# Kernel tuning notes

Hardware: AMD Instinct MI355X
Metric: run time of the kernel (lower is better)

Reference implementation:

```python
import jax, jax.numpy as jnp
import numpy as np
from jax import lax

B, N, C = 4, 4096, 512
HEADS, SR = 8, 4
HW = 64  # spatial size, HW*HW == N
EPS = 1e-5


def setup_inputs() -> dict:
    key = jax.random.key(0)
    ks = jax.random.split(key, 12)
    s = 0.02
    return {
        "x": jax.random.normal(ks[0], (B, N, C), jnp.float32),
        "wq": jax.random.normal(ks[1], (C, C), jnp.float32) * s,
        "bq": jnp.zeros((C,), jnp.float32),
        "wk": jax.random.normal(ks[2], (C, C), jnp.float32) * s,
        "bk": jnp.zeros((C,), jnp.float32),
        "wv": jax.random.normal(ks[3], (C, C), jnp.float32) * s,
        "bv": jnp.zeros((C,), jnp.float32),
        "w_sr": jax.random.normal(ks[4], (SR, SR, C, C), jnp.float32) * s,  # HWIO
        "b_sr": jnp.zeros((C,), jnp.float32),
        "gamma": jnp.ones((C,), jnp.float32),
        "beta": jnp.zeros((C,), jnp.float32),
        "wp": jax.random.normal(ks[5], (C, C), jnp.float32) * s,
        "bp": jnp.zeros((C,), jnp.float32),
    }


def _layernorm(x, gamma, beta):
    mu = jnp.mean(x, axis=-1, keepdims=True)
    var = jnp.mean(jnp.square(x - mu), axis=-1, keepdims=True)
    return (x - mu) * lax.rsqrt(var + EPS) * gamma + beta


def reference(x, wq, bq, wk, bk, wv, bv, w_sr, b_sr, gamma, beta, wp, bp):
    b, n, c = x.shape
    dh = c // HEADS
    scale = dh ** (-0.5)
    # Q at full resolution: [b, heads, n, dh]
    q = (x @ wq + bq).reshape(b, n, HEADS, dh).transpose(0, 2, 1, 3)
    # spatial reduction of K/V: conv stride=kernel=SR (VALID)
    xr = x.reshape(b, HW, HW, c)
    xr = lax.conv_general_dilated(
        xr, w_sr, window_strides=(SR, SR), padding="VALID",
        dimension_numbers=("NHWC", "HWIO", "NHWC")) + b_sr
    xr = xr.reshape(b, -1, c)  # [b, n_kv, c]
    xr = _layernorm(xr, gamma, beta)
    n_kv = xr.shape[1]
    k = (xr @ wk + bk).reshape(b, n_kv, HEADS, dh).transpose(0, 2, 1, 3)
    v = (xr @ wv + bv).reshape(b, n_kv, HEADS, dh).transpose(0, 2, 1, 3)
    attn = jnp.einsum("bhqd,bhkd->bhqk", q, k) * scale
    attn = jax.nn.softmax(attn, axis=-1)
    out = jnp.einsum("bhqk,bhkd->bhqd", attn, v)
    out = out.transpose(0, 2, 1, 3).reshape(b, n, c)
    return out @ wp + bp
```

## Files before the change

### kernel.cpp

```cpp
#include <hip/hip_runtime.h>
#include <hip/hip_bf16.h>


#define EPSV 1e-5f

typedef __attribute__((ext_vector_type(8))) short short8v;
typedef __attribute__((ext_vector_type(4))) short short4v;
typedef __attribute__((ext_vector_type(4))) float float4v;

static __device__ __forceinline__ ushort f2bf_bits(float x) {
  union { float f; uint32_t u; } v; v.f = x;
  return (ushort)((v.u + 0x7fffu + ((v.u >> 16) & 1u)) >> 16);
}

static __device__ __forceinline__ float4v mfma16(short8v a, short8v b, float4v c) {
  return __builtin_amdgcn_mfma_f32_16x16x32_bf16(a, b, c, 0, 0, 0);
}

static __device__ __forceinline__ void wr_chunk(ushort* lds, int base, int4 v) {
  *(int2*)&lds[base]       = make_int2(v.x, v.y);
  *(int2*)&lds[base + 128] = make_int2(v.z, v.w);
}

__global__ __launch_bounds__(256) void cast_x(const float* __restrict__ src,
                                              ushort* __restrict__ dst) {
  const int i = blockIdx.x * 256 + threadIdx.x;
  const float4* s4 = (const float4*)src;
  const float4 a = s4[2 * i], b = s4[2 * i + 1];
  short8v v;
  v[0] = (short)f2bf_bits(a.x); v[1] = (short)f2bf_bits(a.y);
  v[2] = (short)f2bf_bits(a.z); v[3] = (short)f2bf_bits(a.w);
  v[4] = (short)f2bf_bits(b.x); v[5] = (short)f2bf_bits(b.y);
  v[6] = (short)f2bf_bits(b.z); v[7] = (short)f2bf_bits(b.w);
  *(short8v*)&dst[(size_t)i * 8] = v;
}

__global__ __launch_bounds__(256) void tcast(const float* __restrict__ src,
                                             ushort* __restrict__ dst, int K) {
  const int t = blockIdx.x * 256 + threadIdx.x;
  const int k = t >> 7, n4 = (t & 127) * 4;
  const float4 v = *(const float4*)&src[(size_t)k * 512 + n4];
  dst[(size_t)(n4 + 0) * K + k] = f2bf_bits(v.x);
  dst[(size_t)(n4 + 1) * K + k] = f2bf_bits(v.y);
  dst[(size_t)(n4 + 2) * K + k] = f2bf_bits(v.z);
  dst[(size_t)(n4 + 3) * K + k] = f2bf_bits(v.w);
}

__global__ __launch_bounds__(256) void concat_bias(const float* __restrict__ bk,
                                                   const float* __restrict__ bv,
                                                   float* __restrict__ bkv) {
  const int i = blockIdx.x * 256 + threadIdx.x;
  bkv[i] = (i < 512) ? bk[i] : bv[i - 512];
}

template<int MODE>
__global__ __launch_bounds__(256)
void gemm_bf(const ushort* __restrict__ A, const ushort* __restrict__ BT,
             const float* __restrict__ bias, void* __restrict__ outp,
             int M, int N, int K, float scale) {
  __shared__ ushort lds[8192];
  const int tid = threadIdx.x;
  const int wave = tid >> 6, lane = tid & 63;
  const int wm = wave >> 1, wn = wave & 1;
  const int bm = blockIdx.x * 128, bn = blockIdx.y * 128;
  const int lid = lane & 15, lg = lane >> 4;
  const int r0 = tid >> 2, c8 = tid & 3;
  const int g0 = 2 * (c8 & 1), h2 = c8 >> 1;
  const int c0 = c8 * 8;
  const int basew = ((r0 >> 4) * 64 + 16 * g0 + (r0 & 15)) * 8 + h2 * 4;
  float4v acc[4][4];
  const float4v zf = {0.f, 0.f, 0.f, 0.f};
#pragma unroll
  for (int mi = 0; mi < 4; ++mi)
#pragma unroll
    for (int ni = 0; ni < 4; ++ni) acc[mi][ni] = zf;
  const ushort* Ar0 = A + (size_t)(bm + r0) * K;
  const ushort* Ar1 = Ar0 + (size_t)64 * K;
  const ushort* Br0 = BT + (size_t)(bn + r0) * K;
  const ushort* Br1 = Br0 + (size_t)64 * K;
  const int NK = K >> 5;
  int koff = c0;
  int4 pa0 = *(const int4*)(Ar0 + koff), pa1 = *(const int4*)(Ar1 + koff);
  int4 pb0 = *(const int4*)(Br0 + koff), pb1 = *(const int4*)(Br1 + koff);
  for (int kb = 0; kb < NK; ++kb) {
    wr_chunk(lds, basew, pa0);
    wr_chunk(lds, basew + 2048, pa1);
    wr_chunk(lds, basew + 4096, pb0);
    wr_chunk(lds, basew + 6144, pb1);
    __syncthreads();
    if (kb + 1 < NK) {
      koff += 32;
      pa0 = *(const int4*)(Ar0 + koff); pa1 = *(const int4*)(Ar1 + koff);
      pb0 = *(const int4*)(Br0 + koff); pb1 = *(const int4*)(Br1 + koff);
    }
    short8v af[4], bfr[4];
#pragma unroll
    for (int mi = 0; mi < 4; ++mi)
      af[mi] = *(const short8v*)&lds[((wm * 4 + mi) * 64 + lane) * 8];
#pragma unroll
    for (int ni = 0; ni < 4; ++ni)
      bfr[ni] = *(const short8v*)&lds[4096 + ((wn * 4 + ni) * 64 + lane) * 8];
#pragma unroll
    for (int mi = 0; mi < 4; ++mi)
#pragma unroll
      for (int ni = 0; ni < 4; ++ni) acc[mi][ni] = mfma16(af[mi], bfr[ni], acc[mi][ni]);
    __syncthreads();
  }
  float bv[4];
#pragma unroll
  for (int ni = 0; ni < 4; ++ni) bv[ni] = bias[bn + wn * 64 + ni * 16 + lid];
#pragma unroll
  for (int mi = 0; mi < 4; ++mi)
#pragma unroll
    for (int ni = 0; ni < 4; ++ni) {
      const int col = bn + wn * 64 + ni * 16 + lid;
#pragma unroll
      for (int reg = 0; reg < 4; ++reg) {
        const int row = bm + wm * 64 + mi * 16 + 4 * lg + reg;
        const float v = (acc[mi][ni][reg] + bv[ni]) * scale;
        if (MODE == 0) ((float*)outp)[(size_t)row * N + col] = v;
        else if (MODE == 1) ((ushort*)outp)[(size_t)row * N + col] = f2bf_bits(v);
        else {
          if (col < 512) ((ushort*)outp)[(size_t)row * 512 + col] = f2bf_bits(v);
          else ((ushort*)outp)[524288 + (size_t)(col - 512) * 1024 + row] = f2bf_bits(v);
        }
      }
    }
}

static __device__ __forceinline__ int4 ld_patch(const ushort* xbf, int b, int oh, int ow, int kg) {
  const int ij = kg >> 9, ci = kg & 511;
  const int n = (oh * 4 + (ij >> 2)) * 64 + ow * 4 + (ij & 3);
  return *(const int4*)(xbf + ((size_t)b * 4096 + n) * 512 + ci);
}

__global__ __launch_bounds__(256)
void conv_bf(const ushort* __restrict__ xbf, const ushort* __restrict__ wsrT,
             float* __restrict__ part) {
  __shared__ ushort lds[8192];
  const int tid = threadIdx.x;
  const int wave = tid >> 6, lane = tid & 63;
  const int wm = wave >> 1, wn = wave & 1;
  const int bm = blockIdx.x * 128, bn = blockIdx.y * 128, z = blockIdx.z;
  const int lid = lane & 15, lg = lane >> 4;
  const int r0 = tid >> 2, c8 = tid & 3;
  const int g0 = 2 * (c8 & 1), h2 = c8 >> 1;
  const int c0 = c8 * 8;
  const int basew = ((r0 >> 4) * 64 + 16 * g0 + (r0 & 15)) * 8 + h2 * 4;
  const int p0 = bm + r0, p1 = p0 + 64;
  const int b0 = p0 >> 8, oh0 = (p0 & 255) >> 4, ow0 = p0 & 15;
  const int b1 = p1 >> 8, oh1 = (p1 & 255) >> 4, ow1 = p1 & 15;
  const ushort* Br0 = wsrT + (size_t)(bn + r0) * 8192;
  const ushort* Br1 = Br0 + (size_t)64 * 8192;
  float4v acc[4][4];
  const float4v zf = {0.f, 0.f, 0.f, 0.f};
#pragma unroll
  for (int mi = 0; mi < 4; ++mi)
#pragma unroll
    for (int ni = 0; ni < 4; ++ni) acc[mi][ni] = zf;
  int kg = z * 1024 + c0;
  int4 pa0 = ld_patch(xbf, b0, oh0, ow0, kg);
  int4 pa1 = ld_patch(xbf, b1, oh1, ow1, kg);
  int4 pb0 = *(const int4*)(Br0 + kg);
  int4 pb1 = *(const int4*)(Br1 + kg);
  for (int kb = 0; kb < 32; ++kb) {
    wr_chunk(lds, basew, pa0);
    wr_chunk(lds, basew + 2048, pa1);
    wr_chunk(lds, basew + 4096, pb0);
    wr_chunk(lds, basew + 6144, pb1);
    __syncthreads();
    if (kb < 31) {
      kg += 32;
      pa0 = ld_patch(xbf, b0, oh0, ow0, kg);
      pa1 = ld_patch(xbf, b1, oh1, ow1, kg);
      pb0 = *(const int4*)(Br0 + kg);
      pb1 = *(const int4*)(Br1 + kg);
    }
    short8v af[4], bfr[4];
#pragma unroll
    for (int mi = 0; mi < 4; ++mi)
      af[mi] = *(const short8v*)&lds[((wm * 4 + mi) * 64 + lane) * 8];
#pragma unroll
    for (int ni = 0; ni < 4; ++ni)
      bfr[ni] = *(const short8v*)&lds[4096 + ((wn * 4 + ni) * 64 + lane) * 8];
#pragma unroll
    for (int mi = 0; mi < 4; ++mi)
#pragma unroll
      for (int ni = 0; ni < 4; ++ni) acc[mi][ni] = mfma16(af[mi], bfr[ni], acc[mi][ni]);
    __syncthreads();
  }
#pragma unroll
  for (int mi = 0; mi < 4; ++mi)
#pragma unroll
    for (int ni = 0; ni < 4; ++ni)
#pragma unroll
      for (int reg = 0; reg < 4; ++reg)
        part[(size_t)(z * 1024 + bm + wm * 64 + mi * 16 + 4 * lg + reg) * 512 +
             bn + wn * 64 + ni * 16 + lid] = acc[mi][ni][reg];
}

__global__ __launch_bounds__(256)
void reduce_ln(const float* __restrict__ part, const float* __restrict__ bsr,
               const float* __restrict__ gamma, const float* __restrict__ beta,
               ushort* __restrict__ xln) {
  const int wave = threadIdx.x >> 6;
  const int lane = threadIdx.x & 63;
  const int row = blockIdx.x * 4 + wave;
  const int c = lane * 8;
  float v[8];
  {
    const float4 a = *(const float4*)&bsr[c];
    const float4 b = *(const float4*)&bsr[c + 4];
    v[0] = a.x; v[1] = a.y; v[2] = a.z; v[3] = a.w;
    v[4] = b.x; v[5] = b.y; v[6] = b.z; v[7] = b.w;
  }
#pragma unroll
  for (int z = 0; z < 8; ++z) {
    const float* pr = &part[((size_t)z * 1024 + row) * 512 + c];
    const float4 a = *(const float4*)pr;
    const float4 b = *(const float4*)(pr + 4);
    v[0] += a.x; v[1] += a.y; v[2] += a.z; v[3] += a.w;
    v[4] += b.x; v[5] += b.y; v[6] += b.z; v[7] += b.w;
  }
  float sum = 0.f;
#pragma unroll
  for (int i = 0; i < 8; ++i) sum += v[i];
#pragma unroll
  for (int off = 32; off >= 1; off >>= 1) sum += __shfl_xor(sum, off);
  const float mu = sum * (1.0f / 512.0f);
  float sq = 0.f;
#pragma unroll
  for (int i = 0; i < 8; ++i) { v[i] -= mu; sq += v[i] * v[i]; }
#pragma unroll
  for (int off = 32; off >= 1; off >>= 1) sq += __shfl_xor(sq, off);
  const float rs = rsqrtf(sq * (1.0f / 512.0f) + EPSV);
  const float4 g1 = *(const float4*)&gamma[c];
  const float4 g2 = *(const float4*)&gamma[c + 4];
  const float4 e1 = *(const float4*)&beta[c];
  const float4 e2 = *(const float4*)&beta[c + 4];
  const float g[8] = {g1.x, g1.y, g1.z, g1.w, g2.x, g2.y, g2.z, g2.w};
  const float e[8] = {e1.x, e1.y, e1.z, e1.w, e2.x, e2.y, e2.z, e2.w};
  short8v ov;
#pragma unroll
  for (int i = 0; i < 8; ++i) ov[i] = (short)f2bf_bits(v[i] * rs * g[i] + e[i]);
  *(short8v*)&xln[(size_t)row * 512 + c] = ov;
}

__global__ __launch_bounds__(256)
void attn_bf(const ushort* __restrict__ qbf, const ushort* __restrict__ kbf,
             const ushort* __restrict__ vt, ushort* __restrict__ attno) {
  __shared__ ushort kv_lds[16384];
  const int bh = blockIdx.x, qt = blockIdx.y;
  const int b = bh >> 3, h = bh & 7;
  const int tid = threadIdx.x;
  const int wave = tid >> 6, lane = tid & 63;
  const int lid = lane & 15, lg = lane >> 4;
  {
    const ushort* Kb = kbf + (size_t)(b * 256) * 512 + h * 64;
#pragma unroll
    for (int i = 0; i < 8; ++i) {
      const int u = i * 256 + tid;
      const int kv = u >> 3, c8 = u & 7, d0 = c8 * 8;
      const int4 d = *(const int4*)(Kb + (size_t)kv * 512 + d0);
      const int f = (kv >> 4) * 2 + (d0 >> 5);
      const int g0 = (d0 >> 2) & 3, hh2 = (d0 >> 4) & 1;
      wr_chunk(kv_lds, (f * 64 + 16 * g0 + (kv & 15)) * 8 + hh2 * 4, d);
    }
  }
  short8v qfr[2][2];
  const int qrow0 = qt * 128 + wave * 32;
#pragma unroll
  for (int qf = 0; qf < 2; ++qf)
#pragma unroll
    for (int t = 0; t < 2; ++t) {
      const size_t base = (size_t)(b * 4096 + qrow0 + qf * 16 + lid) * 512 + h * 64 + 32 * t + 4 * lg;
      const short4v lo = *(const short4v*)&qbf[base];
      const short4v hi = *(const short4v*)&qbf[base + 16];
      short8v q;
      q[0] = lo[0]; q[1] = lo[1]; q[2] = lo[2]; q[3] = lo[3];
      q[4] = hi[0]; q[5] = hi[1]; q[6] = hi[2]; q[7] = hi[3];
      qfr[qf][t] = q;
    }
  __syncthreads();
  float4v s[16][2];
  const float4v zf = {0.f, 0.f, 0.f, 0.f};
#pragma unroll
  for (int kvf = 0; kvf < 16; ++kvf) { s[kvf][0] = zf; s[kvf][1] = zf; }
#pragma unroll
  for (int kvf = 0; kvf < 16; ++kvf)
#pragma unroll
    for (int t = 0; t < 2; ++t) {
      const short8v ka = *(const short8v*)&kv_lds[((kvf * 2 + t) * 64 + lane) * 8];
      s[kvf][0] = mfma16(ka, qfr[0][t], s[kvf][0]);
      s[kvf][1] = mfma16(ka, qfr[1][t], s[kvf][1]);
    }
  float inv[2];
#pragma unroll
  for (int qf = 0; qf < 2; ++qf) {
    float m = -1e30f;
#pragma unroll
    for (int kvf = 0; kvf < 16; ++kvf)
#pragma unroll
      for (int e = 0; e < 4; ++e) m = fmaxf(m, s[kvf][qf][e]);
    m = fmaxf(m, __shfl_xor(m, 16));
    m = fmaxf(m, __shfl_xor(m, 32));
    float sum = 0.f;
#pragma unroll
    for (int kvf = 0; kvf < 16; ++kvf)
#pragma unroll
      for (int e = 0; e < 4; ++e) {
        const float p = __expf(s[kvf][qf][e] - m);
        s[kvf][qf][e] = p;
        sum += p;
      }
    sum += __shfl_xor(sum, 16);
    sum += __shfl_xor(sum, 32);
    inv[qf] = 1.0f / sum;
  }
  __syncthreads();
  {
    const ushort* Vb = vt + (size_t)(h * 64) * 1024 + b * 256;
#pragma unroll
    for (int i = 0; i < 8; ++i) {
      const int u = i * 256 + tid;
      const int d = u >> 5, c8 = u & 31, kv0 = c8 * 8;
      const int4 dd = *(const int4*)(Vb + (size_t)d * 1024 + kv0);
      const int f = (d >> 4) * 8 + (kv0 >> 5);
      const int g0 = (kv0 >> 2) & 3, hh2 = (kv0 >> 4) & 1;
      wr_chunk(kv_lds, (f * 64 + 16 * g0 + (d & 15)) * 8 + hh2 * 4, dd);
    }
  }
  __syncthreads();
  float4v o[2][4];
#pragma unroll
  for (int qf = 0; qf < 2; ++qf)
#pragma unroll
    for (int nf = 0; nf < 4; ++nf) o[qf][nf] = zf;
#pragma unroll
  for (int t = 0; t < 8; ++t) {
    short8v vb[4];
#pragma unroll
    for (int nf = 0; nf < 4; ++nf)
      vb[nf] = *(const short8v*)&kv_lds[((nf * 8 + t) * 64 + lane) * 8];
#pragma unroll
    for (int qf = 0; qf < 2; ++qf) {
      short8v pa;
#pragma unroll
      for (int j = 0; j < 4; ++j) {
        pa[j]     = (short)f2bf_bits(s[2 * t][qf][j] * inv[qf]);
        pa[4 + j] = (short)f2bf_bits(s[2 * t + 1][qf][j] * inv[qf]);
      }
#pragma unroll
      for (int nf = 0; nf < 4; ++nf) o[qf][nf] = mfma16(pa, vb[nf], o[qf][nf]);
    }
  }
#pragma unroll
  for (int qf = 0; qf < 2; ++qf)
#pragma unroll
    for (int nf = 0; nf < 4; ++nf)
#pragma unroll
      for (int reg = 0; reg < 4; ++reg) {
        const int q = qrow0 + qf * 16 + 4 * lg + reg;
        const int c = h * 64 + nf * 16 + lid;
        attno[(size_t)(b * 4096 + q) * 512 + c] = f2bf_bits(o[qf][nf][reg]);
      }
}

extern "C" void kernel_launch(void* const* d_in, const int* in_sizes, int n_in,
                              void* d_out, int out_size, void* d_ws, size_t ws_size,
                              hipStream_t stream) {
  const float* x     = (const float*)d_in[0];
  const float* wq    = (const float*)d_in[1];
  const float* bq    = (const float*)d_in[2];
  const float* wk    = (const float*)d_in[3];
  const float* bk    = (const float*)d_in[4];
  const float* wv    = (const float*)d_in[5];
  const float* bv    = (const float*)d_in[6];
  const float* wsr   = (const float*)d_in[7];
  const float* bsr   = (const float*)d_in[8];
  const float* gamma = (const float*)d_in[9];
  const float* beta  = (const float*)d_in[10];
  const float* wp    = (const float*)d_in[11];
  const float* bp    = (const float*)d_in[12];
  float* out = (float*)d_out;

  char* w = (char*)d_ws;
  ushort* xbf   = (ushort*)(w);
  ushort* qbf   = (ushort*)(w + 16777216);
  ushort* attno = (ushort*)(w + 33554432);
  float*  part  = (float*) (w + 33554432);
  ushort* wsrT  = (ushort*)(w + 50331648);
  ushort* wqT   = (ushort*)(w + 58720256);
  ushort* wpT   = (ushort*)(w + 59244544);
  ushort* wkvT  = (ushort*)(w + 59768832);
  ushort* xln   = (ushort*)(w + 60817408);
  ushort* kbf   = (ushort*)(w + 61865984);
  ushort* vt    = (ushort*)(w + 62914560);
  float*  bkv   = (float*) (w + 63963136);

  cast_x<<<4096, 256, 0, stream>>>(x, xbf);
  tcast<<<256, 256, 0, stream>>>(wq, wqT, 512);
  tcast<<<256, 256, 0, stream>>>(wk, wkvT, 512);
  tcast<<<256, 256, 0, stream>>>(wv, wkvT + 512 * 512, 512);
  tcast<<<256, 256, 0, stream>>>(wp, wpT, 512);
  tcast<<<4096, 256, 0, stream>>>(wsr, wsrT, 8192);
  concat_bias<<<4, 256, 0, stream>>>(bk, bv, bkv);

  conv_bf<<<dim3(8, 4, 8), 256, 0, stream>>>(xbf, wsrT, part);
  reduce_ln<<<256, 256, 0, stream>>>(part, bsr, gamma, beta, xln);
  gemm_bf<2><<<dim3(8, 8), 256, 0, stream>>>(xln, wkvT, bkv, kbf, 1024, 1024, 512, 1.0f);
  gemm_bf<1><<<dim3(128, 4), 256, 0, stream>>>(xbf, wqT, bq, qbf, 16384, 512, 512, 0.125f);
  attn_bf<<<dim3(32, 32), 256, 0, stream>>>(qbf, kbf, vt, attno);
  gemm_bf<0><<<dim3(128, 4), 256, 0, stream>>>(attno, wpT, bp, out, 16384, 512, 512, 1.0f);
}
```

Measured before the change: 262.1 us.

## Fuse prep kernels, split conv K wider, use exp2 softmax and deferred normalization

Merges the x cast, the weight transposes and the bias concat into one prep launch. Doubles the conv split-K factor (16 partial sums) so more blocks run, at the cost of more partial traffic for reduce_ln to read. Folds log2(e) into the Q scale so softmax can use the native exp2, and moves the 1/sum normalization from the P operand to the output epilogue via shuffles. Also switches the bf16 conversion to the library intrinsic.

Result: faster. 241.1 us (-8.0%).

```diff
diff --git a/kernel.cpp b/kernel.cpp
--- a/kernel.cpp
+++ b/kernel.cpp
@@ -3,14 +3,15 @@
 
 
 #define EPSV 1e-5f
+#define SCALE_Q 0.18033688011112042f
 
 typedef __attribute__((ext_vector_type(8))) short short8v;
 typedef __attribute__((ext_vector_type(4))) short short4v;
 typedef __attribute__((ext_vector_type(4))) float float4v;
 
 static __device__ __forceinline__ ushort f2bf_bits(float x) {
-  union { float f; uint32_t u; } v; v.f = x;
-  return (ushort)((v.u + 0x7fffu + ((v.u >> 16) & 1u)) >> 16);
+  __hip_bfloat16 h = __float2bfloat16(x);
+  return *(ushort*)&h;
 }
 
 static __device__ __forceinline__ float4v mfma16(short8v a, short8v b, float4v c) {
@@ -22,35 +23,48 @@
   *(int2*)&lds[base + 128] = make_int2(v.z, v.w);
 }
 
-__global__ __launch_bounds__(256) void cast_x(const float* __restrict__ src,
-                                              ushort* __restrict__ dst) {
-  const int i = blockIdx.x * 256 + threadIdx.x;
-  const float4* s4 = (const float4*)src;
-  const float4 a = s4[2 * i], b = s4[2 * i + 1];
-  short8v v;
-  v[0] = (short)f2bf_bits(a.x); v[1] = (short)f2bf_bits(a.y);
-  v[2] = (short)f2bf_bits(a.z); v[3] = (short)f2bf_bits(a.w);
-  v[4] = (short)f2bf_bits(b.x); v[5] = (short)f2bf_bits(b.y);
-  v[6] = (short)f2bf_bits(b.z); v[7] = (short)f2bf_bits(b.w);
-  *(short8v*)&dst[(size_t)i * 8] = v;
-}
-
-__global__ __launch_bounds__(256) void tcast(const float* __restrict__ src,
-                                             ushort* __restrict__ dst, int K) {
-  const int t = blockIdx.x * 256 + threadIdx.x;
-  const int k = t >> 7, n4 = (t & 127) * 4;
-  const float4 v = *(const float4*)&src[(size_t)k * 512 + n4];
-  dst[(size_t)(n4 + 0) * K + k] = f2bf_bits(v.x);
-  dst[(size_t)(n4 + 1) * K + k] = f2bf_bits(v.y);
-  dst[(size_t)(n4 + 2) * K + k] = f2bf_bits(v.z);
-  dst[(size_t)(n4 + 3) * K + k] = f2bf_bits(v.w);
-}
-
-__global__ __launch_bounds__(256) void concat_bias(const float* __restrict__ bk,
-                                                   const float* __restrict__ bv,
-                                                   float* __restrict__ bkv) {
-  const int i = blockIdx.x * 256 + threadIdx.x;
-  bkv[i] = (i < 512) ? bk[i] : bv[i - 512];
+__global__ __launch_bounds__(256)
+void prep(const float* __restrict__ x, const float* __restrict__ wq,
+          const float* __restrict__ wk, const float* __restrict__ wv,
+          const float* __restrict__ wp, const float* __restrict__ wsr,
+          const float* __restrict__ bk, const float* __restrict__ bv,
+          ushort* __restrict__ xbf, ushort* __restrict__ wqT,
+          ushort* __restrict__ wkvT, ushort* __restrict__ wpT,
+          ushort* __restrict__ wsrT, float* __restrict__ bkv) {
+  const int bid = blockIdx.x, tid = threadIdx.x;
+  if (bid < 4096) {
+    const int i = bid * 256 + tid;
+    const float4* s4 = (const float4*)x;
+    const float4 a = s4[2 * i], b = s4[2 * i + 1];
+    short8v v;
+    v[0] = (short)f2bf_bits(a.x); v[1] = (short)f2bf_bits(a.y);
+    v[2] = (short)f2bf_bits(a.z); v[3] = (short)f2bf_bits(a.w);
+    v[4] = (short)f2bf_bits(b.x); v[5] = (short)f2bf_bits(b.y);
+    v[6] = (short)f2bf_bits(b.z); v[7] = (short)f2bf_bits(b.w);
+    *(short8v*)&xbf[(size_t)i * 8] = v;
+  } else if (bid < 8192) {
+    const int t = (bid - 4096) * 256 + tid;
+    const int k = t >> 7, n4 = (t & 127) * 4;
+    const float4 v = *(const float4*)&wsr[(size_t)k * 512 + n4];
+    wsrT[(size_t)(n4 + 0) * 8192 + k] = f2bf_bits(v.x);
+    wsrT[(size_t)(n4 + 1) * 8192 + k] = f2bf_bits(v.y);
+    wsrT[(size_t)(n4 + 2) * 8192 + k] = f2bf_bits(v.z);
+    wsrT[(size_t)(n4 + 3) * 8192 + k] = f2bf_bits(v.w);
+  } else if (bid < 9216) {
+    const int wsel = (bid - 8192) >> 8;
+    const int t = ((bid - 8192) & 255) * 256 + tid;
+    const float* src = wsel == 0 ? wq : wsel == 1 ? wk : wsel == 2 ? wv : wp;
+    ushort* dst = wsel == 0 ? wqT : wsel == 1 ? wkvT : wsel == 2 ? (wkvT + 262144) : wpT;
+    const int k = t >> 7, n4 = (t & 127) * 4;
+    const float4 v = *(const float4*)&src[(size_t)k * 512 + n4];
+    dst[(size_t)(n4 + 0) * 512 + k] = f2bf_bits(v.x);
+    dst[(size_t)(n4 + 1) * 512 + k] = f2bf_bits(v.y);
+    dst[(size_t)(n4 + 2) * 512 + k] = f2bf_bits(v.z);
+    dst[(size_t)(n4 + 3) * 512 + k] = f2bf_bits(v.w);
+  } else {
+    const int i = (bid - 9216) * 256 + tid;
+    bkv[i] = (i < 512) ? bk[i] : bv[i - 512];
+  }
 }
 
 template<int MODE>
@@ -106,9 +120,9 @@
       for (int ni = 0; ni < 4; ++ni) acc[mi][ni] = mfma16(af[mi], bfr[ni], acc[mi][ni]);
     __syncthreads();
   }
-  float bv[4];
-#pragma unroll
-  for (int ni = 0; ni < 4; ++ni) bv[ni] = bias[bn + wn * 64 + ni * 16 + lid];
+  float bvv[4];
+#pragma unroll
+  for (int ni = 0; ni < 4; ++ni) bvv[ni] = bias[bn + wn * 64 + ni * 16 + lid];
 #pragma unroll
   for (int mi = 0; mi < 4; ++mi)
 #pragma unroll
@@ -117,7 +131,7 @@
 #pragma unroll
       for (int reg = 0; reg < 4; ++reg) {
         const int row = bm + wm * 64 + mi * 16 + 4 * lg + reg;
-        const float v = (acc[mi][ni][reg] + bv[ni]) * scale;
+        const float v = (acc[mi][ni][reg] + bvv[ni]) * scale;
         if (MODE == 0) ((float*)outp)[(size_t)row * N + col] = v;
         else if (MODE == 1) ((ushort*)outp)[(size_t)row * N + col] = f2bf_bits(v);
         else {
@@ -158,18 +172,18 @@
   for (int mi = 0; mi < 4; ++mi)
 #pragma unroll
     for (int ni = 0; ni < 4; ++ni) acc[mi][ni] = zf;
-  int kg = z * 1024 + c0;
+  int kg = z * 512 + c0;
   int4 pa0 = ld_patch(xbf, b0, oh0, ow0, kg);
   int4 pa1 = ld_patch(xbf, b1, oh1, ow1, kg);
   int4 pb0 = *(const int4*)(Br0 + kg);
   int4 pb1 = *(const int4*)(Br1 + kg);
-  for (int kb = 0; kb < 32; ++kb) {
+  for (int kb = 0; kb < 16; ++kb) {
     wr_chunk(lds, basew, pa0);
     wr_chunk(lds, basew + 2048, pa1);
     wr_chunk(lds, basew + 4096, pb0);
     wr_chunk(lds, basew + 6144, pb1);
     __syncthreads();
-    if (kb < 31) {
+    if (kb < 15) {
       kg += 32;
       pa0 = ld_patch(xbf, b0, oh0, ow0, kg);
       pa1 = ld_patch(xbf, b1, oh1, ow1, kg);
@@ -215,7 +229,7 @@
     v[4] = b.x; v[5] = b.y; v[6] = b.z; v[7] = b.w;
   }
 #pragma unroll
-  for (int z = 0; z < 8; ++z) {
+  for (int z = 0; z < 16; ++z) {
     const float* pr = &part[((size_t)z * 1024 + row) * 512 + c];
     const float4 a = *(const float4*)pr;
     const float4 b = *(const float4*)(pr + 4);
@@ -309,7 +323,7 @@
     for (int kvf = 0; kvf < 16; ++kvf)
 #pragma unroll
       for (int e = 0; e < 4; ++e) {
-        const float p = __expf(s[kvf][qf][e] - m);
+        const float p = __builtin_amdgcn_exp2f(s[kvf][qf][e] - m);
         s[kvf][qf][e] = p;
         sum += p;
       }
@@ -347,23 +361,27 @@
       short8v pa;
 #pragma unroll
       for (int j = 0; j < 4; ++j) {
-        pa[j]     = (short)f2bf_bits(s[2 * t][qf][j] * inv[qf]);
-        pa[4 + j] = (short)f2bf_bits(s[2 * t + 1][qf][j] * inv[qf]);
+        pa[j]     = (short)f2bf_bits(s[2 * t][qf][j]);
+        pa[4 + j] = (short)f2bf_bits(s[2 * t + 1][qf][j]);
       }
 #pragma unroll
       for (int nf = 0; nf < 4; ++nf) o[qf][nf] = mfma16(pa, vb[nf], o[qf][nf]);
     }
   }
 #pragma unroll
-  for (int qf = 0; qf < 2; ++qf)
+  for (int qf = 0; qf < 2; ++qf) {
+    float sc[4];
+#pragma unroll
+    for (int reg = 0; reg < 4; ++reg) sc[reg] = __shfl(inv[qf], 4 * lg + reg);
 #pragma unroll
     for (int nf = 0; nf < 4; ++nf)
 #pragma unroll
       for (int reg = 0; reg < 4; ++reg) {
         const int q = qrow0 + qf * 16 + 4 * lg + reg;
         const int c = h * 64 + nf * 16 + lid;
-        attno[(size_t)(b * 4096 + q) * 512 + c] = f2bf_bits(o[qf][nf][reg]);
+        attno[(size_t)(b * 4096 + q) * 512 + c] = f2bf_bits(o[qf][nf][reg] * sc[reg]);
       }
+  }
 }
 
 extern "C" void kernel_launch(void* const* d_in, const int* in_sizes, int n_in,
@@ -388,28 +406,22 @@
   ushort* xbf   = (ushort*)(w);
   ushort* qbf   = (ushort*)(w + 16777216);
   ushort* attno = (ushort*)(w + 33554432);
-  float*  part  = (float*) (w + 33554432);
-  ushort* wsrT  = (ushort*)(w + 50331648);
-  ushort* wqT   = (ushort*)(w + 58720256);
-  ushort* wpT   = (ushort*)(w + 59244544);
-  ushort* wkvT  = (ushort*)(w + 59768832);
-  ushort* xln   = (ushort*)(w + 60817408);
-  ushort* kbf   = (ushort*)(w + 61865984);
-  ushort* vt    = (ushort*)(w + 62914560);
-  float*  bkv   = (float*) (w + 63963136);
-
-  cast_x<<<4096, 256, 0, stream>>>(x, xbf);
-  tcast<<<256, 256, 0, stream>>>(wq, wqT, 512);
-  tcast<<<256, 256, 0, stream>>>(wk, wkvT, 512);
-  tcast<<<256, 256, 0, stream>>>(wv, wkvT + 512 * 512, 512);
-  tcast<<<256, 256, 0, stream>>>(wp, wpT, 512);
-  tcast<<<4096, 256, 0, stream>>>(wsr, wsrT, 8192);
-  concat_bias<<<4, 256, 0, stream>>>(bk, bv, bkv);
-
-  conv_bf<<<dim3(8, 4, 8), 256, 0, stream>>>(xbf, wsrT, part);
+  float*  part  = (float*) (w + 50331648);
+  ushort* wsrT  = (ushort*)(w + 83886080);
+  ushort* wqT   = (ushort*)(w + 92274688);
+  ushort* wpT   = (ushort*)(w + 92798976);
+  ushort* wkvT  = (ushort*)(w + 93323264);
+  ushort* xln   = (ushort*)(w + 94371840);
+  ushort* kbf   = (ushort*)(w + 95420416);
+  ushort* vt    = (ushort*)(w + 96468992);
+  float*  bkv   = (float*) (w + 97517568);
+
+  prep<<<9220, 256, 0, stream>>>(x, wq, wk, wv, wp, wsr, bk, bv,
+                                 xbf, wqT, wkvT, wpT, wsrT, bkv);
+  conv_bf<<<dim3(8, 4, 16), 256, 0, stream>>>(xbf, wsrT, part);
   reduce_ln<<<256, 256, 0, stream>>>(part, bsr, gamma, beta, xln);
   gemm_bf<2><<<dim3(8, 8), 256, 0, stream>>>(xln, wkvT, bkv, kbf, 1024, 1024, 512, 1.0f);
-  gemm_bf<1><<<dim3(128, 4), 256, 0, stream>>>(xbf, wqT, bq, qbf, 16384, 512, 512, 0.125f);
+  gemm_bf<1><<<dim3(128, 4), 256, 0, stream>>>(xbf, wqT, bq, qbf, 16384, 512, 512, SCALE_Q);
   attn_bf<<<dim3(32, 32), 256, 0, stream>>>(qbf, kbf, vt, attno);
   gemm_bf<0><<<dim3(128, 4), 256, 0, stream>>>(attno, wpT, bp, out, 16384, 512, 512, 1.0f);
 }
```
